# Optimization experiments

Hardware: AMD Instinct MI355X
Metric: run time of the kernel (lower is better)

## Reference

```python
import jax, jax.numpy as jnp
import numpy as np

V, S, D, H, F, LYR, NLAB, B = 30522, 512, 768, 12, 3072, 12, 2, 16
DH = D // H
EPS = 1e-5


def layer_norm(x, scale, bias):
    mu = jnp.mean(x, axis=-1, keepdims=True)
    var = jnp.mean((x - mu) ** 2, axis=-1, keepdims=True)
    return (x - mu) * jax.lax.rsqrt(var + EPS) * scale + bias


def setup_inputs() -> dict:
    key = jax.random.key(0)
    ks = jax.random.split(key, 16)
    sc = 0.02
    inp = {
        "input_ids": jax.random.randint(ks[0], (B, S), 0, V),
        "token_emb": jax.random.normal(ks[1], (V, D), jnp.float32) * sc,
        "pos_emb": jax.random.normal(ks[2], (S, D), jnp.float32) * sc,
        "emb_ln_s": jnp.ones((D,), jnp.float32),
        "emb_ln_b": jnp.zeros((D,), jnp.float32),
        "wq": jax.random.normal(ks[3], (LYR, H, D, DH), jnp.float32) * sc,
        "wk": jax.random.normal(ks[4], (LYR, H, D, DH), jnp.float32) * sc,
        "wv": jax.random.normal(ks[5], (LYR, H, D, DH), jnp.float32) * sc,
        "wo": jax.random.normal(ks[6], (LYR, D, D), jnp.float32) * sc,
        "wo_b": jnp.zeros((LYR, D), jnp.float32),
        "ln1_s": jnp.ones((LYR, D), jnp.float32),
        "ln1_b": jnp.zeros((LYR, D), jnp.float32),
        "ln2_s": jnp.ones((LYR, D), jnp.float32),
        "ln2_b": jnp.zeros((LYR, D), jnp.float32),
        "ff1_w": jax.random.normal(ks[7], (LYR, D, F), jnp.float32) * sc,
        "ff1_b": jnp.zeros((LYR, F), jnp.float32),
        "ff2_w": jax.random.normal(ks[8], (LYR, F, D), jnp.float32) * sc,
        "ff2_b": jnp.zeros((LYR, D), jnp.float32),
        "final_ln_s": jnp.ones((D,), jnp.float32),
        "final_ln_b": jnp.zeros((D,), jnp.float32),
        "clf_w": jax.random.normal(ks[9], (D, NLAB), jnp.float32) * sc,
        "clf_b": jnp.zeros((NLAB,), jnp.float32),
    }
    return inp


def _encoder_block(x, wq, wk, wv, wo, wo_b, ln1_s, ln1_b, ln2_s, ln2_b,
                   ff1_w, ff1_b, ff2_w, ff2_b):
    # pre-LN attention with residual
    h = layer_norm(x, ln1_s, ln1_b)
    q = jnp.einsum("bsd,hde->bhse", h, wq)
    k = jnp.einsum("bsd,hde->bhse", h, wk)
    v = jnp.einsum("bsd,hde->bhse", h, wv)
    scores = jnp.einsum("bhse,bhte->bhst", q, k) / jnp.sqrt(jnp.float32(DH))
    # NOTE: source uses log_softmax (quirk), faithfully preserved
    w = jax.nn.log_softmax(scores, axis=-1)
    ctx = jnp.einsum("bhst,bhte->bhse", w, v)
    ctx = ctx.transpose(0, 2, 1, 3).reshape(x.shape[0], x.shape[1], D)
    x = x + ctx @ wo + wo_b
    # pre-LN FFN with residual (exact GELU as in torch nn.GELU)
    h2 = layer_norm(x, ln2_s, ln2_b)
    ff = jax.nn.gelu(h2 @ ff1_w + ff1_b, approximate=False) @ ff2_w + ff2_b
    return x + ff


def reference(input_ids, token_emb, pos_emb, emb_ln_s, emb_ln_b,
              wq, wk, wv, wo, wo_b, ln1_s, ln1_b, ln2_s, ln2_b,
              ff1_w, ff1_b, ff2_w, ff2_b, final_ln_s, final_ln_b,
              clf_w, clf_b):
    x = token_emb[input_ids] + pos_emb[None, :, :]
    x = layer_norm(x, emb_ln_s, emb_ln_b)
    for l in range(LYR):
        x = _encoder_block(x, wq[l], wk[l], wv[l], wo[l], wo_b[l],
                           ln1_s[l], ln1_b[l], ln2_s[l], ln2_b[l],
                           ff1_w[l], ff1_b[l], ff2_w[l], ff2_b[l])
    x = layer_norm(x, final_ln_s, final_ln_b)
    cls = x[:, 0, :]
    return cls @ clf_w + clf_b
```

## Files before the change

### kernel.cpp

```cpp
#include <hip/hip_runtime.h>
#include <hip/hip_bf16.h>
#include <math.h>

typedef __bf16 bf16_t;
typedef __attribute__((ext_vector_type(8))) __bf16 bf16x8;
typedef __attribute__((ext_vector_type(4))) float f32x4;

typedef const __attribute__((address_space(1))) void av1_void;
typedef __attribute__((address_space(3))) void av3_void;

#define DEV static __device__ __forceinline__

DEV void gload16(const void* g, void* l) {
  __builtin_amdgcn_global_load_lds((av1_void*)g, (av3_void*)l, 16, 0, 0);
}

DEV float bsum3(float v, float* red) {
#pragma unroll
  for (int o = 32; o > 0; o >>= 1) v += __shfl_xor(v, o, 64);
  __syncthreads();
  if ((threadIdx.x & 63) == 0) red[threadIdx.x >> 6] = v;
  __syncthreads();
  return red[0] + red[1] + red[2];
}

__global__ __launch_bounds__(192) void k_embed(
    const int* __restrict__ ids, const float* __restrict__ tok,
    const float* __restrict__ pos, const float* __restrict__ gam,
    const float* __restrict__ bet, const float* __restrict__ gam2,
    const float* __restrict__ bet2, float* __restrict__ x,
    bf16_t* __restrict__ h) {
  __shared__ float red[3];
  int row = blockIdx.x;
  int s = row & 511;
  int t = threadIdx.x;
  int id = ids[row];
  const float4 tv = *(const float4*)&tok[(size_t)id * 768 + t * 4];
  const float4 pv = *(const float4*)&pos[(size_t)s * 768 + t * 4];
  float v[4] = {tv.x + pv.x, tv.y + pv.y, tv.z + pv.z, tv.w + pv.w};
  float tot = bsum3(v[0] + v[1] + v[2] + v[3], red);
  float mu = tot * (1.f / 768.f);
  float sq = 0.f;
#pragma unroll
  for (int u = 0; u < 4; ++u) { float d = v[u] - mu; sq += d * d; }
  float var = bsum3(sq, red) * (1.f / 768.f);
  float rstd = rsqrtf(var + 1e-5f);
  const float4 g4 = *(const float4*)&gam[t * 4];
  const float4 b4 = *(const float4*)&bet[t * 4];
  float o[4];
  o[0] = (v[0] - mu) * rstd * g4.x + b4.x;
  o[1] = (v[1] - mu) * rstd * g4.y + b4.y;
  o[2] = (v[2] - mu) * rstd * g4.z + b4.z;
  o[3] = (v[3] - mu) * rstd * g4.w + b4.w;
  float4 ov = {o[0], o[1], o[2], o[3]};
  *(float4*)&x[(size_t)row * 768 + t * 4] = ov;
  float tot2 = bsum3(o[0] + o[1] + o[2] + o[3], red);
  float mu2 = tot2 * (1.f / 768.f);
  float sq2 = 0.f;
#pragma unroll
  for (int u = 0; u < 4; ++u) { float d = o[u] - mu2; sq2 += d * d; }
  float var2 = bsum3(sq2, red) * (1.f / 768.f);
  float rstd2 = rsqrtf(var2 + 1e-5f);
  const float4 G = *(const float4*)&gam2[t * 4];
  const float4 Bb = *(const float4*)&bet2[t * 4];
  union { bf16_t ob[4]; uint2 u2; } pk;
  pk.ob[0] = (bf16_t)((o[0] - mu2) * rstd2 * G.x + Bb.x);
  pk.ob[1] = (bf16_t)((o[1] - mu2) * rstd2 * G.y + Bb.y);
  pk.ob[2] = (bf16_t)((o[2] - mu2) * rstd2 * G.z + Bb.z);
  pk.ob[3] = (bf16_t)((o[3] - mu2) * rstd2 * G.w + Bb.w);
  *(uint2*)&h[(size_t)row * 768 + t * 4] = pk.u2;
}

__global__ __launch_bounds__(256) void k_ln(
    const float* __restrict__ xin, bf16_t* __restrict__ hout,
    const float* __restrict__ gam, const float* __restrict__ bet) {
  int row = blockIdx.x * 4 + (threadIdx.x >> 6);
  int lane = threadIdx.x & 63;
  const float* xr = xin + (size_t)row * 768 + lane * 12;
  float4 a = *(const float4*)&xr[0];
  float4 b = *(const float4*)&xr[4];
  float4 c = *(const float4*)&xr[8];
  float v[12] = {a.x, a.y, a.z, a.w, b.x, b.y, b.z, b.w, c.x, c.y, c.z, c.w};
  float sm = 0.f;
#pragma unroll
  for (int u = 0; u < 12; ++u) sm += v[u];
#pragma unroll
  for (int o = 32; o > 0; o >>= 1) sm += __shfl_xor(sm, o, 64);
  float mu = sm * (1.f / 768.f);
  float sq = 0.f;
#pragma unroll
  for (int u = 0; u < 12; ++u) { float d = v[u] - mu; sq += d * d; }
#pragma unroll
  for (int o = 32; o > 0; o >>= 1) sq += __shfl_xor(sq, o, 64);
  float rstd = rsqrtf(sq * (1.f / 768.f) + 1e-5f);
  const float4 ga = *(const float4*)&gam[lane * 12];
  const float4 gb = *(const float4*)&gam[lane * 12 + 4];
  const float4 gc = *(const float4*)&gam[lane * 12 + 8];
  const float4 ba = *(const float4*)&bet[lane * 12];
  const float4 bb = *(const float4*)&bet[lane * 12 + 4];
  const float4 bc = *(const float4*)&bet[lane * 12 + 8];
  float g[12] = {ga.x, ga.y, ga.z, ga.w, gb.x, gb.y, gb.z, gb.w,
                 gc.x, gc.y, gc.z, gc.w};
  float be[12] = {ba.x, ba.y, ba.z, ba.w, bb.x, bb.y, bb.z, bb.w,
                  bc.x, bc.y, bc.z, bc.w};
  union { bf16_t o[12]; uint2 u2[3]; } pk;
#pragma unroll
  for (int u = 0; u < 12; ++u)
    pk.o[u] = (bf16_t)((v[u] - mu) * rstd * g[u] + be[u]);
  bf16_t* hr = hout + (size_t)row * 768 + lane * 12;
#pragma unroll
  for (int u = 0; u < 3; ++u) *(uint2*)&hr[u * 4] = pk.u2[u];
}

__global__ __launch_bounds__(256) void k_convT(
    const float* __restrict__ in, size_t in_slice, bf16_t* __restrict__ out,
    size_t out_slice, int N, int K) {
  __shared__ float tbuf[32][33];
  int slice = blockIdx.z;
  const float* ip = in + (size_t)slice * in_slice;
  bf16_t* op = out + (size_t)slice * out_slice;
  int n0 = blockIdx.x * 32, k0 = blockIdx.y * 32;
  int c = threadIdx.x & 31, r8 = threadIdx.x >> 5;
#pragma unroll
  for (int i = 0; i < 4; ++i) {
    int rr = r8 + i * 8;
    tbuf[rr][c] = ip[(size_t)(k0 + rr) * N + n0 + c];
  }
  __syncthreads();
#pragma unroll
  for (int i = 0; i < 4; ++i) {
    int rr = r8 + i * 8;
    op[(size_t)(n0 + rr) * K + k0 + c] = (bf16_t)tbuf[c][rr];
  }
}

__global__ __launch_bounds__(256) void k_convT3(
    const float* __restrict__ wq, const float* __restrict__ wk,
    const float* __restrict__ wv, bf16_t* __restrict__ out,
    size_t in_lstride, size_t out_lstride) {
  __shared__ float tbuf[32][33];
  int z = blockIdx.z;
  int l = z / 36, r = z % 36;
  int which = r / 12, head = r % 12;
  const float* ip = (which == 0 ? wq : which == 1 ? wk : wv) +
                    (size_t)l * in_lstride + (size_t)head * 768 * 64;
  bf16_t* op = out + (size_t)l * out_lstride + (size_t)which * 768 * 768 +
               (size_t)head * 64 * 768;
  int n0 = blockIdx.x * 32, k0 = blockIdx.y * 32;
  int c = threadIdx.x & 31, r8 = threadIdx.x >> 5;
#pragma unroll
  for (int i = 0; i < 4; ++i) {
    int rr = r8 + i * 8;
    tbuf[rr][c] = ip[(size_t)(k0 + rr) * 64 + n0 + c];
  }
  __syncthreads();
#pragma unroll
  for (int i = 0; i < 4; ++i) {
    int rr = r8 + i * 8;
    op[(size_t)(n0 + rr) * 768 + k0 + c] = (bf16_t)tbuf[c][rr];
  }
}

template <int EPI>
__global__ __launch_bounds__(256) void k_gemm1(
    const bf16_t* __restrict__ A, int lda, const bf16_t* __restrict__ Bt,
    int ldb, int K, float* __restrict__ Cf, bf16_t* __restrict__ Cb, int ldc,
    const float* __restrict__ bias, int gx) {
  __shared__ __attribute__((aligned(16))) bf16_t As[128 * 64];
  __shared__ __attribute__((aligned(16))) bf16_t Bs[128 * 64];
  const int nwg = gridDim.x;
  const int bid = blockIdx.x;
  const int cpx = nwg >> 3;
  const int swz = (bid & 7) * cpx + (bid >> 3);
  const int bx = swz % gx, by = swz / gx;
  const int m0 = by << 7, n0 = bx << 7;
  const int tid = threadIdx.x;
  const int lane = tid & 63, w = tid >> 6;
  const int wm = w >> 1, wn = w & 1;
  const int r = lane & 15, g4 = lane >> 4;

  f32x4 acc[4][4];
#pragma unroll
  for (int m = 0; m < 4; ++m)
#pragma unroll
    for (int n = 0; n < 4; ++n)
#pragma unroll
      for (int e = 0; e < 4; ++e) acc[m][n][e] = 0.f;

  const bf16_t* pa[4];
  const bf16_t* pb[4];
  char* la[4];
  char* lb[4];
#pragma unroll
  for (int u = 0; u < 4; ++u) {
    int s = u * 256 + tid;
    int row = s >> 3;
    int c = (s & 7) ^ (row & 7);
    pa[u] = A + (size_t)(m0 + row) * lda + c * 8;
    pb[u] = Bt + (size_t)(n0 + row) * ldb + c * 8;
    la[u] = (char*)As + (size_t)(u * 256 + (w << 6)) * 16;
    lb[u] = (char*)Bs + (size_t)(u * 256 + (w << 6)) * 16;
  }

  const int NT = K >> 6;
  for (int t = 0; t < NT; ++t) {
    const int k0 = t << 6;
#pragma unroll
    for (int u = 0; u < 4; ++u) gload16(pa[u] + k0, la[u]);
#pragma unroll
    for (int u = 0; u < 4; ++u) gload16(pb[u] + k0, lb[u]);
    __syncthreads();

#pragma unroll
    for (int kk = 0; kk < 2; ++kk) {
      bf16x8 af[4], bb[4];
#pragma unroll
      for (int m = 0; m < 4; ++m) {
        int row = wm * 64 + m * 16 + r;
        af[m] = *(const bf16x8*)&As[row * 64 +
                                    (((kk << 2) + g4) ^ (row & 7)) * 8];
      }
#pragma unroll
      for (int n = 0; n < 4; ++n) {
        int row = wn * 64 + n * 16 + r;
        bb[n] = *(const bf16x8*)&Bs[row * 64 +
                                    (((kk << 2) + g4) ^ (row & 7)) * 8];
      }
#pragma unroll
      for (int m = 0; m < 4; ++m)
#pragma unroll
        for (int n = 0; n < 4; ++n)
          acc[m][n] = __builtin_amdgcn_mfma_f32_16x16x32_bf16(af[m], bb[n],
                                                              acc[m][n], 0, 0, 0);
    }
    __syncthreads();
  }

#pragma unroll
  for (int m = 0; m < 4; ++m) {
#pragma unroll
    for (int n = 0; n < 4; ++n) {
      int col = n0 + wn * 64 + n * 16 + r;
      float bv = 0.f;
      if constexpr (EPI != 0) bv = bias[col];
#pragma unroll
      for (int j = 0; j < 4; ++j) {
        int row = m0 + wm * 64 + m * 16 + g4 * 4 + j;
        float v = acc[m][n][j];
        if constexpr (EPI == 0) {
          Cb[(size_t)row * ldc + col] = (bf16_t)v;
        } else if constexpr (EPI == 1) {
          size_t o = (size_t)row * ldc + col;
          Cf[o] += v + bv;
        } else {
          float tt = v + bv;
          float ge = 0.5f * tt * (1.f + erff(tt * 0.70710678118f));
          Cb[(size_t)row * ldc + col] = (bf16_t)ge;
        }
      }
    }
  }
}

template <int EPI>
__global__ __launch_bounds__(256) void k_gemm3(
    const bf16_t* __restrict__ A, int lda, const bf16_t* __restrict__ Bt,
    int ldb, int K, float* __restrict__ Cf, bf16_t* __restrict__ Cb, int ldc,
    const float* __restrict__ bias, int gx) {
  __shared__ __attribute__((aligned(16))) bf16_t As[3][128 * 32];
  __shared__ __attribute__((aligned(16))) bf16_t Bs[3][128 * 32];
  const int nwg = gridDim.x;
  const int bid = blockIdx.x;
  const int cpx = nwg >> 3;
  const int swz = (bid & 7) * cpx + (bid >> 3);
  const int bx = swz % gx, by = swz / gx;
  const int m0 = by << 7, n0 = bx << 7;
  const int tid = threadIdx.x;
  const int lane = tid & 63, w = tid >> 6;
  const int wm = w >> 1, wn = w & 1;
  const int r = lane & 15, g4 = lane >> 4;

  f32x4 acc[4][4];
#pragma unroll
  for (int m = 0; m < 4; ++m)
#pragma unroll
    for (int n = 0; n < 4; ++n)
#pragma unroll
      for (int e = 0; e < 4; ++e) acc[m][n][e] = 0.f;

  const bf16_t* pa[2];
  const bf16_t* pb[2];
  uint32_t lo[2];
#pragma unroll
  for (int u = 0; u < 2; ++u) {
    int s = u * 256 + tid;
    int row = s >> 2;
    int c = (s & 3) ^ ((row >> 1) & 3);
    pa[u] = A + (size_t)(m0 + row) * lda + c * 8;
    pb[u] = Bt + (size_t)(n0 + row) * ldb + c * 8;
    lo[u] = (uint32_t)(u * 256 + (w << 6)) * 16;
  }

  const int NT = K >> 5;
  auto STAGE = [&](int t, int bufi) {
    int k0 = (t < NT ? t : NT - 1) << 5;
#pragma unroll
    for (int u = 0; u < 2; ++u) gload16(pa[u] + k0, (char*)&As[bufi][0] + lo[u]);
#pragma unroll
    for (int u = 0; u < 2; ++u) gload16(pb[u] + k0, (char*)&Bs[bufi][0] + lo[u]);
  };

  STAGE(0, 0);
  STAGE(1, 1);
  int bi = 0, si = 2;
  const int co = (g4 ^ ((r >> 1) & 3)) << 3;
  for (int t = 0; t < NT; ++t) {
    asm volatile("s_waitcnt vmcnt(4)" ::: "memory");
    asm volatile("s_barrier" ::: "memory");
    bf16x8 af[4], bb[4];
#pragma unroll
    for (int m = 0; m < 4; ++m) {
      int row = wm * 64 + m * 16 + r;
      af[m] = *(const bf16x8*)&As[bi][row * 32 + co];
    }
#pragma unroll
    for (int n = 0; n < 4; ++n) {
      int row = wn * 64 + n * 16 + r;
      bb[n] = *(const bf16x8*)&Bs[bi][row * 32 + co];
    }
#pragma unroll
    for (int m = 0; m < 4; ++m)
#pragma unroll
      for (int n = 0; n < 4; ++n)
        acc[m][n] = __builtin_amdgcn_mfma_f32_16x16x32_bf16(af[m], bb[n],
                                                            acc[m][n], 0, 0, 0);
    asm volatile("s_barrier" ::: "memory");
    STAGE(t + 2, si);
    si = bi;
    bi = (bi == 2) ? 0 : bi + 1;
  }
  asm volatile("s_waitcnt vmcnt(0)" ::: "memory");

#pragma unroll
  for (int m = 0; m < 4; ++m) {
#pragma unroll
    for (int n = 0; n < 4; ++n) {
      int col = n0 + wn * 64 + n * 16 + r;
      float bv = 0.f;
      if constexpr (EPI != 0) bv = bias[col];
#pragma unroll
      for (int j = 0; j < 4; ++j) {
        int row = m0 + wm * 64 + m * 16 + g4 * 4 + j;
        float v = acc[m][n][j];
        if constexpr (EPI == 0) {
          Cb[(size_t)row * ldc + col] = (bf16_t)v;
        } else if constexpr (EPI == 1) {
          size_t o = (size_t)row * ldc + col;
          Cf[o] += v + bv;
        } else {
          float tt = v + bv;
          float ge = 0.5f * tt * (1.f + erff(tt * 0.70710678118f));
          Cb[(size_t)row * ldc + col] = (bf16_t)ge;
        }
      }
    }
  }
}

__global__ __launch_bounds__(256) void k_lse(const bf16_t* __restrict__ qkv,
                                             float* __restrict__ lseb) {
  __shared__ __attribute__((aligned(16))) bf16_t Ks[512 * 64];
  __shared__ __attribute__((aligned(16))) bf16_t Qs[64 * 64];
  int bh = blockIdx.x;
  int b = bh / 12, hh = bh % 12;
  int s0 = blockIdx.y * 64;
  int tid = threadIdx.x, lane = tid & 63, w = tid >> 6;
  int r = lane & 15, g4 = lane >> 4;
  const bf16_t* kb = qkv + (size_t)b * 512 * 2304 + 768 + hh * 64;
  const bf16_t* qb = qkv + ((size_t)(b * 512 + s0)) * 2304 + hh * 64;
#pragma unroll
  for (int i = 0; i < 16; ++i) {
    int c = i * 256 + tid;
    gload16(kb + (size_t)(c >> 3) * 2304 + (c & 7) * 8,
            (char*)Ks + (size_t)(i * 256 + (w << 6)) * 16);
  }
#pragma unroll
  for (int i = 0; i < 2; ++i) {
    int c = i * 256 + tid;
    gload16(qb + (size_t)(c >> 3) * 2304 + (c & 7) * 8,
            (char*)Qs + (size_t)(i * 256 + (w << 6)) * 16);
  }
  __syncthreads();

  f32x4 acc[32];
#pragma unroll
  for (int n = 0; n < 32; ++n)
#pragma unroll
    for (int e = 0; e < 4; ++e) acc[n][e] = 0.f;

#pragma unroll
  for (int kk = 0; kk < 2; ++kk) {
    bf16x8 aq = *(const bf16x8*)&Qs[(w * 16 + r) * 64 + kk * 32 + g4 * 8];
#pragma unroll
    for (int n = 0; n < 32; ++n) {
      bf16x8 bk = *(const bf16x8*)&Ks[(n * 16 + r) * 64 + kk * 32 + g4 * 8];
      acc[n] = __builtin_amdgcn_mfma_f32_16x16x32_bf16(aq, bk, acc[n], 0, 0, 0);
    }
  }
#pragma unroll
  for (int j = 0; j < 4; ++j) {
    float mx = -1e30f;
#pragma unroll
    for (int n = 0; n < 32; ++n) mx = fmaxf(mx, acc[n][j] * 0.125f);
#pragma unroll
    for (int o = 1; o < 16; o <<= 1) mx = fmaxf(mx, __shfl_xor(mx, o, 64));
    float sm = 0.f;
#pragma unroll
    for (int n = 0; n < 32; ++n) sm += expf(acc[n][j] * 0.125f - mx);
#pragma unroll
    for (int o = 1; o < 16; o <<= 1) sm += __shfl_xor(sm, o, 64);
    if (r == 0)
      lseb[(size_t)bh * 512 + s0 + w * 16 + g4 * 4 + j] = mx + logf(sm);
  }
}

__global__ __launch_bounds__(256) void k_attn2(
    const bf16_t* __restrict__ qkv, const float* __restrict__ lseb,
    bf16_t* __restrict__ ctx) {
  __shared__ __attribute__((aligned(16))) char arena[65536];
  __shared__ __attribute__((aligned(16))) bf16_t Mt[64 * 64];
  __shared__ float svs[64];
  bf16_t* Ks = (bf16_t*)arena;
  float* Vs = (float*)(arena + 16384);
  bf16_t* Qs = (bf16_t*)arena;

  int bh = blockIdx.x;
  int b = bh / 12, hh = bh % 12;
  int tid = threadIdx.x, lane = tid & 63, w = tid >> 6;
  const bf16_t* kb = qkv + (size_t)b * 512 * 2304 + 768 + hh * 64;
  const bf16_t* vb = qkv + (size_t)b * 512 * 2304 + 1536 + hh * 64;
  const bf16_t* qb = qkv + (size_t)b * 512 * 2304 + hh * 64;

  int e1 = lane, grp = w;
  f32x4 macc[4];
#pragma unroll
  for (int jj = 0; jj < 4; ++jj)
#pragma unroll
    for (int e = 0; e < 4; ++e) macc[jj][e] = 0.f;
  float sv = 0.f;

  for (int t0 = 0; t0 < 512; t0 += 128) {
#pragma unroll
    for (int i = 0; i < 4; ++i) {
      int c = i * 256 + tid;
      gload16(kb + (size_t)(t0 + (c >> 3)) * 2304 + (c & 7) * 8,
              (char*)Ks + (size_t)(i * 256 + (w << 6)) * 16);
    }
#pragma unroll
    for (int i = 0; i < 4; ++i) {
      int c = i * 256 + tid;
      int row = c >> 3, col = (c & 7) * 8;
      bf16x8 raw = *(const bf16x8*)(vb + (size_t)(t0 + row) * 2304 + col);
      f32x4 v0, v1;
#pragma unroll
      for (int u = 0; u < 4; ++u) { v0[u] = (float)raw[u]; v1[u] = (float)raw[u + 4]; }
      *(f32x4*)&Vs[row * 64 + col] = v0;
      *(f32x4*)&Vs[row * 64 + col + 4] = v1;
    }
    __syncthreads();
    for (int tt = 0; tt < 128; ++tt) {
      float kv = (float)Ks[tt * 64 + e1];
#pragma unroll
      for (int jj = 0; jj < 4; ++jj) {
        f32x4 vv = *(const f32x4*)&Vs[tt * 64 + grp * 16 + jj * 4];
        macc[jj] += kv * vv;
      }
    }
    if (tid < 64) {
      for (int tt = 0; tt < 128; ++tt) sv += Vs[tt * 64 + tid];
    }
    __syncthreads();
  }
#pragma unroll
  for (int jj = 0; jj < 4; ++jj)
#pragma unroll
    for (int u = 0; u < 4; ++u)
      Mt[(grp * 16 + jj * 4 + u) * 64 + e1] = (bf16_t)(macc[jj][u] * 0.125f);
  if (tid < 64) svs[tid] = sv;
  __syncthreads();

  int r = lane & 15, g4 = lane >> 4;
#pragma unroll
  for (int i = 0; i < 16; ++i) {
    int c = i * 256 + tid;
    gload16(qb + (size_t)(c >> 3) * 2304 + (c & 7) * 8,
            (char*)Qs + (size_t)(i * 256 + (w << 6)) * 16);
  }
  __syncthreads();

  f32x4 acc[8][4];
#pragma unroll
  for (int m = 0; m < 8; ++m)
#pragma unroll
    for (int n = 0; n < 4; ++n)
#pragma unroll
      for (int e = 0; e < 4; ++e) acc[m][n][e] = 0.f;

#pragma unroll
  for (int kk = 0; kk < 2; ++kk) {
    bf16x8 bm[4];
#pragma unroll
    for (int n = 0; n < 4; ++n)
      bm[n] = *(const bf16x8*)&Mt[(n * 16 + r) * 64 + kk * 32 + g4 * 8];
#pragma unroll
    for (int m = 0; m < 8; ++m) {
      bf16x8 aq = *(const bf16x8*)&Qs[(w * 128 + m * 16 + r) * 64 + kk * 32 + g4 * 8];
#pragma unroll
      for (int n = 0; n < 4; ++n)
        acc[m][n] = __builtin_amdgcn_mfma_f32_16x16x32_bf16(aq, bm[n], acc[m][n], 0, 0, 0);
    }
  }
#pragma unroll
  for (int m = 0; m < 8; ++m) {
#pragma unroll
    for (int n = 0; n < 4; ++n) {
      int col = n * 16 + r;
      float svv = svs[col];
#pragma unroll
      for (int j = 0; j < 4; ++j) {
        int s = w * 128 + m * 16 + g4 * 4 + j;
        float lv = lseb[(size_t)bh * 512 + s];
        float val = acc[m][n][j] - lv * svv;
        ctx[((size_t)(b * 512 + s)) * 768 + hh * 64 + col] = (bf16_t)val;
      }
    }
  }
}

__global__ __launch_bounds__(192) void k_final(
    const float* __restrict__ x, const float* __restrict__ gam,
    const float* __restrict__ bet, const float* __restrict__ cw,
    const float* __restrict__ cb, float* __restrict__ out) {
  __shared__ float red[3];
  int b = blockIdx.x, t = threadIdx.x;
  const float* xr = x + (size_t)b * 512 * 768;
  const float4 xv = *(const float4*)&xr[t * 4];
  float v[4] = {xv.x, xv.y, xv.z, xv.w};
  float tot = bsum3(v[0] + v[1] + v[2] + v[3], red);
  float mu = tot * (1.f / 768.f);
  float sq = 0.f;
#pragma unroll
  for (int u = 0; u < 4; ++u) { float d = v[u] - mu; sq += d * d; }
  float var = bsum3(sq, red) * (1.f / 768.f);
  float rstd = rsqrtf(var + 1e-5f);
  const float4 g4 = *(const float4*)&gam[t * 4];
  const float4 b4 = *(const float4*)&bet[t * 4];
  float nv[4];
  nv[0] = (v[0] - mu) * rstd * g4.x + b4.x;
  nv[1] = (v[1] - mu) * rstd * g4.y + b4.y;
  nv[2] = (v[2] - mu) * rstd * g4.z + b4.z;
  nv[3] = (v[3] - mu) * rstd * g4.w + b4.w;
  const float4 wa = *(const float4*)&cw[t * 8];
  const float4 wb = *(const float4*)&cw[t * 8 + 4];
  float d0 = nv[0] * wa.x + nv[1] * wa.z + nv[2] * wb.x + nv[3] * wb.z;
  float d1 = nv[0] * wa.y + nv[1] * wa.w + nv[2] * wb.y + nv[3] * wb.w;
  d0 = bsum3(d0, red);
  d1 = bsum3(d1, red);
  if (t == 0) {
    out[b * 2 + 0] = d0 + cb[0];
    out[b * 2 + 1] = d1 + cb[1];
  }
}

static constexpr size_t OFF_X = 0;
static constexpr size_t OFF_H = OFF_X + 8192ull * 768 * 4;
static constexpr size_t OFF_QG = OFF_H + 8192ull * 768 * 2;
static constexpr size_t OFF_CTX = OFF_QG + 8192ull * 3072 * 2;
static constexpr size_t OFF_LSE = OFF_CTX + 8192ull * 768 * 2;
static constexpr size_t OFF_W = OFF_LSE + 192ull * 512 * 4;
static constexpr size_t WPL = 7077888;
static constexpr size_t WS_SMALL = OFF_W + WPL * 2;
static constexpr size_t WS_BIG = OFF_W + 12ull * WPL * 2;

extern "C" void kernel_launch(void* const* d_in, const int* in_sizes, int n_in,
                              void* d_out, int out_size, void* d_ws,
                              size_t ws_size, hipStream_t stream) {
  const int* ids = (const int*)d_in[0];
  const float* tok = (const float*)d_in[1];
  const float* pos = (const float*)d_in[2];
  const float* eln_s = (const float*)d_in[3];
  const float* eln_b = (const float*)d_in[4];
  const float* wq = (const float*)d_in[5];
  const float* wk = (const float*)d_in[6];
  const float* wv = (const float*)d_in[7];
  const float* wo = (const float*)d_in[8];
  const float* wo_b = (const float*)d_in[9];
  const float* ln1_s = (const float*)d_in[10];
  const float* ln1_b = (const float*)d_in[11];
  const float* ln2_s = (const float*)d_in[12];
  const float* ln2_b = (const float*)d_in[13];
  const float* ff1w = (const float*)d_in[14];
  const float* ff1b = (const float*)d_in[15];
  const float* ff2w = (const float*)d_in[16];
  const float* ff2b = (const float*)d_in[17];
  const float* fln_s = (const float*)d_in[18];
  const float* fln_b = (const float*)d_in[19];
  const float* cw = (const float*)d_in[20];
  const float* cb = (const float*)d_in[21];
  float* out = (float*)d_out;

  if (ws_size < WS_SMALL) return;
  const bool big = ws_size >= WS_BIG;

  char* ws = (char*)d_ws;
  float* x = (float*)(ws + OFF_X);
  bf16_t* h = (bf16_t*)(ws + OFF_H);
  bf16_t* qkv = (bf16_t*)(ws + OFF_QG);
  bf16_t* gbuf = (bf16_t*)(ws + OFF_QG);
  bf16_t* ctx = (bf16_t*)(ws + OFF_CTX);
  float* lseb = (float*)(ws + OFF_LSE);
  bf16_t* wT = (bf16_t*)(ws + OFF_W);

  k_embed<<<8192, 192, 0, stream>>>(ids, tok, pos, eln_s, eln_b,
                                    ln1_s, ln1_b, x, h);

  if (big) {
    k_convT3<<<dim3(2, 24, 432), 256, 0, stream>>>(wq, wk, wv, wT,
                                                   589824, WPL);
    k_convT<<<dim3(24, 24, 12), 256, 0, stream>>>(wo, 589824,
                                                  wT + 1769472, WPL, 768, 768);
    k_convT<<<dim3(96, 24, 12), 256, 0, stream>>>(ff1w, 2359296,
                                                  wT + 2359296, WPL, 3072, 768);
    k_convT<<<dim3(24, 96, 12), 256, 0, stream>>>(ff2w, 2359296,
                                                  wT + 4718592, WPL, 768, 3072);
  }

  for (int l = 0; l < 12; ++l) {
    bf16_t* wl = big ? wT + (size_t)l * WPL : wT;
    bf16_t* qkvT = wl;
    bf16_t* woT = wl + 1769472;
    bf16_t* ff1T = wl + 2359296;
    bf16_t* ff2T = wl + 4718592;

    if (l > 0)
      k_ln<<<2048, 256, 0, stream>>>(x, h, ln1_s + l * 768, ln1_b + l * 768);
    if (!big) {
      k_convT3<<<dim3(2, 24, 36), 256, 0, stream>>>(
          wq + (size_t)l * 589824, wk + (size_t)l * 589824,
          wv + (size_t)l * 589824, qkvT, 589824, 0);
      k_convT<<<dim3(24, 24, 1), 256, 0, stream>>>(wo + (size_t)l * 589824, 0,
                                                   woT, 0, 768, 768);
      k_convT<<<dim3(96, 24, 1), 256, 0, stream>>>(ff1w + (size_t)l * 2359296,
                                                   0, ff1T, 0, 3072, 768);
      k_convT<<<dim3(24, 96, 1), 256, 0, stream>>>(ff2w + (size_t)l * 2359296,
                                                   0, ff2T, 0, 768, 3072);
    }
    k_gemm1<0><<<1152, 256, 0, stream>>>(h, 768, qkvT, 768, 768,
                                         nullptr, qkv, 2304, nullptr, 18);
    k_lse<<<dim3(192, 8), 256, 0, stream>>>(qkv, lseb);
    k_attn2<<<192, 256, 0, stream>>>(qkv, lseb, ctx);
    k_gemm3<1><<<384, 256, 0, stream>>>(ctx, 768, woT, 768, 768, x,
                                        nullptr, 768, wo_b + l * 768, 6);
    k_ln<<<2048, 256, 0, stream>>>(x, h, ln2_s + l * 768, ln2_b + l * 768);
    k_gemm1<2><<<1536, 256, 0, stream>>>(h, 768, ff1T, 768, 768,
                                         nullptr, gbuf, 3072,
                                         ff1b + l * 3072, 24);
    k_gemm3<1><<<384, 256, 0, stream>>>(gbuf, 3072, ff2T, 3072, 3072, x,
                                        nullptr, 768, ff2b + l * 768, 6);
  }
  k_final<<<16, 192, 0, stream>>>(x, fln_s, fln_b, cw, cb, out);
}
```

Before: 4.075 ms.

## Fuse LSE computation into attention kernel with double-buffered Q chunks and swizzled LDS

Merges the separate log-sum-exp kernel into the attention kernel. Each block keeps the full K tile resident in LDS and loops over Q chunks, computing scores, LSE and the output together, with double-buffered Q staging. XOR swizzling is added to LDS layouts to reduce bank conflicts, and the V column sum is split across all waves. This removes one launch, the lseb round trip and the repeated K loads, but reduces the number of parallel blocks for the score/LSE work from 1536 to 192 and increases LDS usage.

```diff
diff --git a/kernel.cpp b/kernel.cpp
--- a/kernel.cpp
+++ b/kernel.cpp
@@ -367,99 +367,46 @@
   }
 }
 
-__global__ __launch_bounds__(256) void k_lse(const bf16_t* __restrict__ qkv,
-                                             float* __restrict__ lseb) {
+__global__ __launch_bounds__(256) void k_attn(const bf16_t* __restrict__ qkv,
+                                              bf16_t* __restrict__ ctx) {
   __shared__ __attribute__((aligned(16))) bf16_t Ks[512 * 64];
-  __shared__ __attribute__((aligned(16))) bf16_t Qs[64 * 64];
-  int bh = blockIdx.x;
-  int b = bh / 12, hh = bh % 12;
-  int s0 = blockIdx.y * 64;
-  int tid = threadIdx.x, lane = tid & 63, w = tid >> 6;
-  int r = lane & 15, g4 = lane >> 4;
-  const bf16_t* kb = qkv + (size_t)b * 512 * 2304 + 768 + hh * 64;
-  const bf16_t* qb = qkv + ((size_t)(b * 512 + s0)) * 2304 + hh * 64;
-#pragma unroll
-  for (int i = 0; i < 16; ++i) {
-    int c = i * 256 + tid;
-    gload16(kb + (size_t)(c >> 3) * 2304 + (c & 7) * 8,
-            (char*)Ks + (size_t)(i * 256 + (w << 6)) * 16);
-  }
-#pragma unroll
-  for (int i = 0; i < 2; ++i) {
-    int c = i * 256 + tid;
-    gload16(qb + (size_t)(c >> 3) * 2304 + (c & 7) * 8,
-            (char*)Qs + (size_t)(i * 256 + (w << 6)) * 16);
-  }
-  __syncthreads();
-
-  f32x4 acc[32];
-#pragma unroll
-  for (int n = 0; n < 32; ++n)
-#pragma unroll
-    for (int e = 0; e < 4; ++e) acc[n][e] = 0.f;
-
-#pragma unroll
-  for (int kk = 0; kk < 2; ++kk) {
-    bf16x8 aq = *(const bf16x8*)&Qs[(w * 16 + r) * 64 + kk * 32 + g4 * 8];
-#pragma unroll
-    for (int n = 0; n < 32; ++n) {
-      bf16x8 bk = *(const bf16x8*)&Ks[(n * 16 + r) * 64 + kk * 32 + g4 * 8];
-      acc[n] = __builtin_amdgcn_mfma_f32_16x16x32_bf16(aq, bk, acc[n], 0, 0, 0);
-    }
-  }
-#pragma unroll
-  for (int j = 0; j < 4; ++j) {
-    float mx = -1e30f;
-#pragma unroll
-    for (int n = 0; n < 32; ++n) mx = fmaxf(mx, acc[n][j] * 0.125f);
-#pragma unroll
-    for (int o = 1; o < 16; o <<= 1) mx = fmaxf(mx, __shfl_xor(mx, o, 64));
-    float sm = 0.f;
-#pragma unroll
-    for (int n = 0; n < 32; ++n) sm += expf(acc[n][j] * 0.125f - mx);
-#pragma unroll
-    for (int o = 1; o < 16; o <<= 1) sm += __shfl_xor(sm, o, 64);
-    if (r == 0)
-      lseb[(size_t)bh * 512 + s0 + w * 16 + g4 * 4 + j] = mx + logf(sm);
-  }
-}
-
-__global__ __launch_bounds__(256) void k_attn2(
-    const bf16_t* __restrict__ qkv, const float* __restrict__ lseb,
-    bf16_t* __restrict__ ctx) {
-  __shared__ __attribute__((aligned(16))) char arena[65536];
+  __shared__ __attribute__((aligned(16))) float Vs[128 * 64];
+  __shared__ __attribute__((aligned(16))) bf16_t Qs[2][64 * 64];
   __shared__ __attribute__((aligned(16))) bf16_t Mt[64 * 64];
+  __shared__ float svp[4 * 64];
   __shared__ float svs[64];
-  bf16_t* Ks = (bf16_t*)arena;
-  float* Vs = (float*)(arena + 16384);
-  bf16_t* Qs = (bf16_t*)arena;
 
   int bh = blockIdx.x;
   int b = bh / 12, hh = bh % 12;
   int tid = threadIdx.x, lane = tid & 63, w = tid >> 6;
-  const bf16_t* kb = qkv + (size_t)b * 512 * 2304 + 768 + hh * 64;
-  const bf16_t* vb = qkv + (size_t)b * 512 * 2304 + 1536 + hh * 64;
+  int r = lane & 15, g4 = lane >> 4;
   const bf16_t* qb = qkv + (size_t)b * 512 * 2304 + hh * 64;
-
-  int e1 = lane, grp = w;
+  const bf16_t* kb = qb + 768;
+  const bf16_t* vb = qb + 1536;
+
+#pragma unroll
+  for (int i = 0; i < 16; ++i) {
+    int s = i * 256 + tid;
+    int row = s >> 3;
+    int c = (s & 7) ^ (row & 7);
+    gload16(kb + (size_t)row * 2304 + c * 8,
+            (char*)Ks + (size_t)(i * 256 + (w << 6)) * 16);
+  }
+
   f32x4 macc[4];
 #pragma unroll
   for (int jj = 0; jj < 4; ++jj)
 #pragma unroll
     for (int e = 0; e < 4; ++e) macc[jj][e] = 0.f;
-  float sv = 0.f;
+  float svacc = 0.f;
+  const int e1 = lane;
+  const int e1hi = (e1 >> 3), e1lo = (e1 & 7);
 
   for (int t0 = 0; t0 < 512; t0 += 128) {
 #pragma unroll
     for (int i = 0; i < 4; ++i) {
-      int c = i * 256 + tid;
-      gload16(kb + (size_t)(t0 + (c >> 3)) * 2304 + (c & 7) * 8,
-              (char*)Ks + (size_t)(i * 256 + (w << 6)) * 16);
-    }
-#pragma unroll
-    for (int i = 0; i < 4; ++i) {
-      int c = i * 256 + tid;
-      int row = c >> 3, col = (c & 7) * 8;
+      int cs = i * 256 + tid;
+      int row = cs >> 3, col = (cs & 7) * 8;
       bf16x8 raw = *(const bf16x8*)(vb + (size_t)(t0 + row) * 2304 + col);
       f32x4 v0, v1;
 #pragma unroll
@@ -469,69 +416,111 @@
     }
     __syncthreads();
     for (int tt = 0; tt < 128; ++tt) {
-      float kv = (float)Ks[tt * 64 + e1];
+      int t = t0 + tt;
+      float kv = (float)Ks[t * 64 + (((e1hi ^ (t & 7)) << 3) | e1lo)];
 #pragma unroll
       for (int jj = 0; jj < 4; ++jj) {
-        f32x4 vv = *(const f32x4*)&Vs[tt * 64 + grp * 16 + jj * 4];
+        f32x4 vv = *(const f32x4*)&Vs[tt * 64 + w * 16 + jj * 4];
         macc[jj] += kv * vv;
       }
     }
-    if (tid < 64) {
-      for (int tt = 0; tt < 128; ++tt) sv += Vs[tt * 64 + tid];
-    }
+    for (int q = 0; q < 32; ++q)
+      svacc += Vs[((w << 5) + q) * 64 + lane];
     __syncthreads();
   }
+
 #pragma unroll
   for (int jj = 0; jj < 4; ++jj)
 #pragma unroll
-    for (int u = 0; u < 4; ++u)
-      Mt[(grp * 16 + jj * 4 + u) * 64 + e1] = (bf16_t)(macc[jj][u] * 0.125f);
-  if (tid < 64) svs[tid] = sv;
+    for (int u = 0; u < 4; ++u) {
+      int e2 = w * 16 + jj * 4 + u;
+      Mt[e2 * 64 + (((e1hi ^ (e2 & 7)) << 3) | e1lo)] =
+          (bf16_t)(macc[jj][u] * 0.125f);
+    }
+  svp[w * 64 + lane] = svacc;
   __syncthreads();
-
-  int r = lane & 15, g4 = lane >> 4;
-#pragma unroll
-  for (int i = 0; i < 16; ++i) {
-    int c = i * 256 + tid;
-    gload16(qb + (size_t)(c >> 3) * 2304 + (c & 7) * 8,
-            (char*)Qs + (size_t)(i * 256 + (w << 6)) * 16);
-  }
-  __syncthreads();
-
-  f32x4 acc[8][4];
-#pragma unroll
-  for (int m = 0; m < 8; ++m)
+  if (w == 0)
+    svs[lane] = svp[lane] + svp[64 + lane] + svp[128 + lane] + svp[192 + lane];
+
+  auto stageQ = [&](int qc, int bufi) {
+#pragma unroll
+    for (int u = 0; u < 2; ++u) {
+      int s = u * 256 + tid;
+      int row = s >> 3;
+      int c = (s & 7) ^ (row & 7);
+      gload16(qb + (size_t)(qc * 64 + row) * 2304 + c * 8,
+              (char*)&Qs[bufi][0] + (size_t)(u * 256 + (w << 6)) * 16);
+    }
+  };
+  stageQ(0, 0);
+  const int arow = w * 16 + r;
+
+  for (int qc = 0; qc < 8; ++qc) {
+    __syncthreads();
+    if (qc < 7) stageQ(qc + 1, (qc + 1) & 1);
+    const bf16_t* Qb = &Qs[qc & 1][0];
+
+    f32x4 acc2[32];
+#pragma unroll
+    for (int n = 0; n < 32; ++n)
+#pragma unroll
+      for (int e = 0; e < 4; ++e) acc2[n][e] = 0.f;
+
+#pragma unroll
+    for (int kk = 0; kk < 2; ++kk) {
+      bf16x8 aq = *(const bf16x8*)&Qb[arow * 64 +
+                                      (((kk << 2) + g4) ^ (arow & 7)) * 8];
+#pragma unroll
+      for (int n = 0; n < 32; ++n) {
+        int krow = n * 16 + r;
+        bf16x8 bk = *(const bf16x8*)&Ks[krow * 64 +
+                                        (((kk << 2) + g4) ^ (krow & 7)) * 8];
+        acc2[n] = __builtin_amdgcn_mfma_f32_16x16x32_bf16(aq, bk, acc2[n], 0, 0, 0);
+      }
+    }
+
+    float lse_j[4];
+#pragma unroll
+    for (int j = 0; j < 4; ++j) {
+      float mx = -1e30f;
+#pragma unroll
+      for (int n = 0; n < 32; ++n) mx = fmaxf(mx, acc2[n][j] * 0.125f);
+#pragma unroll
+      for (int o = 1; o < 16; o <<= 1) mx = fmaxf(mx, __shfl_xor(mx, o, 64));
+      float sm = 0.f;
+#pragma unroll
+      for (int n = 0; n < 32; ++n) sm += expf(acc2[n][j] * 0.125f - mx);
+#pragma unroll
+      for (int o = 1; o < 16; o <<= 1) sm += __shfl_xor(sm, o, 64);
+      lse_j[j] = mx + logf(sm);
+    }
+
+    f32x4 acc3[4];
 #pragma unroll
     for (int n = 0; n < 4; ++n)
 #pragma unroll
-      for (int e = 0; e < 4; ++e) acc[m][n][e] = 0.f;
-
-#pragma unroll
-  for (int kk = 0; kk < 2; ++kk) {
-    bf16x8 bm[4];
-#pragma unroll
-    for (int n = 0; n < 4; ++n)
-      bm[n] = *(const bf16x8*)&Mt[(n * 16 + r) * 64 + kk * 32 + g4 * 8];
-#pragma unroll
-    for (int m = 0; m < 8; ++m) {
-      bf16x8 aq = *(const bf16x8*)&Qs[(w * 128 + m * 16 + r) * 64 + kk * 32 + g4 * 8];
-#pragma unroll
-      for (int n = 0; n < 4; ++n)
-        acc[m][n] = __builtin_amdgcn_mfma_f32_16x16x32_bf16(aq, bm[n], acc[m][n], 0, 0, 0);
-    }
-  }
-#pragma unroll
-  for (int m = 0; m < 8; ++m) {
-#pragma unroll
-    for (int n = 0; n < 4; ++n) {
-      int col = n * 16 + r;
+      for (int e = 0; e < 4; ++e) acc3[n][e] = 0.f;
+#pragma unroll
+    for (int kk = 0; kk < 2; ++kk) {
+      bf16x8 aq = *(const bf16x8*)&Qb[arow * 64 +
+                                      (((kk << 2) + g4) ^ (arow & 7)) * 8];
+#pragma unroll
+      for (int n2 = 0; n2 < 4; ++n2) {
+        int mrow = n2 * 16 + r;
+        bf16x8 bm = *(const bf16x8*)&Mt[mrow * 64 +
+                                        (((kk << 2) + g4) ^ (mrow & 7)) * 8];
+        acc3[n2] = __builtin_amdgcn_mfma_f32_16x16x32_bf16(aq, bm, acc3[n2], 0, 0, 0);
+      }
+    }
+#pragma unroll
+    for (int n2 = 0; n2 < 4; ++n2) {
+      int col = n2 * 16 + r;
       float svv = svs[col];
 #pragma unroll
       for (int j = 0; j < 4; ++j) {
-        int s = w * 128 + m * 16 + g4 * 4 + j;
-        float lv = lseb[(size_t)bh * 512 + s];
-        float val = acc[m][n][j] - lv * svv;
-        ctx[((size_t)(b * 512 + s)) * 768 + hh * 64 + col] = (bf16_t)val;
+        int srow = qc * 64 + w * 16 + g4 * 4 + j;
+        ctx[((size_t)(b * 512 + srow)) * 768 + hh * 64 + col] =
+            (bf16_t)(acc3[n2][j] - lse_j[j] * svv);
       }
     }
   }
@@ -618,7 +607,6 @@
   bf16_t* qkv = (bf16_t*)(ws + OFF_QG);
   bf16_t* gbuf = (bf16_t*)(ws + OFF_QG);
   bf16_t* ctx = (bf16_t*)(ws + OFF_CTX);
-  float* lseb = (float*)(ws + OFF_LSE);
   bf16_t* wT = (bf16_t*)(ws + OFF_W);
 
   k_embed<<<8192, 192, 0, stream>>>(ids, tok, pos, eln_s, eln_b,
@@ -657,8 +645,7 @@
     }
     k_gemm1<0><<<1152, 256, 0, stream>>>(h, 768, qkvT, 768, 768,
                                          nullptr, qkv, 2304, nullptr, 18);
-    k_lse<<<dim3(192, 8), 256, 0, stream>>>(qkv, lseb);
-    k_attn2<<<192, 256, 0, stream>>>(qkv, lseb, ctx);
+    k_attn<<<192, 256, 0, stream>>>(qkv, ctx);
     k_gemm3<1><<<384, 256, 0, stream>>>(ctx, 768, woT, 768, 768, x,
                                         nullptr, 768, wo_b + l * 768, 6);
     k_ln<<<2048, 256, 0, stream>>>(x, h, ln2_s + l * 768, ln2_b + l * 768);
```

New measurement: 4.007 ms. Within noise of the previous version (-1.7%).
